# Performance work log

Hardware: AMD Instinct MI355X
Metric: run time of the kernel (lower is better)

## Reference

```python
import jax, jax.numpy as jnp
import numpy as np

H = 2048            # hidden_size
HK, HV = 16, 32     # num_k_heads, num_v_heads
DK, DV = 128, 128   # head dims
KEY_DIM = HK * DK   # 2048
VAL_DIM = HV * DV   # 4096
CONV_DIM = 2 * KEY_DIM + VAL_DIM  # 8192
KW = 4              # conv kernel width
CS = 64             # chunk size
B, S = 2, 4096
EPS = 1e-6


def setup_inputs() -> dict:
    key = jax.random.key(0)
    ks = jax.random.split(key, 8)
    sc = lambda n: 1.0 / np.sqrt(n)
    return {
        "hidden_states": jax.random.normal(ks[0], (B, S, H), jnp.float32),
        "W_qkvz": jax.random.normal(ks[1], (H, 2 * KEY_DIM + 2 * VAL_DIM), jnp.float32) * sc(H),
        "W_ba": jax.random.normal(ks[2], (H, 2 * HV), jnp.float32) * sc(H),
        "conv_w": jax.random.normal(ks[3], (CONV_DIM, KW), jnp.float32) * sc(KW),
        "A_log": jnp.log(jax.random.uniform(ks[4], (HV,), jnp.float32, 1.0, 16.0)),
        "dt_bias": jax.random.normal(ks[5], (HV,), jnp.float32) * 0.1,
        "norm_weight": jnp.ones((DV,), jnp.float32),
        "W_out": jax.random.normal(ks[6], (VAL_DIM, H), jnp.float32) * sc(VAL_DIM),
    }


def l2norm(x, eps=1e-6):
    return x * jax.lax.rsqrt(jnp.sum(x * x, -1, keepdims=True) + eps)


def chunk_gated_delta_rule(q, k, v, g, beta):
    # q,k: (B,S,HV,DK); v: (B,S,HV,DV); g,beta: (B,S,HV). S divisible by CS.
    q = l2norm(q)
    k = l2norm(k)
    tr = lambda x: jnp.swapaxes(x, 1, 2).astype(jnp.float32)  # -> (B,H,S,...)
    q, k, v = tr(q), tr(k), tr(v)
    g = jnp.swapaxes(g, 1, 2).astype(jnp.float32)
    beta = jnp.swapaxes(beta, 1, 2).astype(jnp.float32)
    q = q * (1.0 / np.sqrt(DK))
    nc = S // CS
    rs = lambda x: x.reshape(B, HV, nc, CS, x.shape[-1])
    v_beta = v * beta[..., None]
    k_beta = k * beta[..., None]
    q, k, v, k_beta, v_beta = map(rs, (q, k, v, k_beta, v_beta))
    g = jnp.cumsum(g.reshape(B, HV, nc, CS), -1)
    tril = jnp.tril(jnp.ones((CS, CS), bool))
    diff = g[..., :, None] - g[..., None, :]
    decay = jnp.exp(jnp.where(tril, diff, 0.0)) * tril  # (B,H,nc,CS,CS)
    # strictly-lower A; the original sequential loop computes T = (I - A)^{-1}
    A = -jnp.tril(jnp.einsum('bhcid,bhcjd->bhcij', k_beta, k) * decay, -1)
    eye = jnp.eye(CS, dtype=jnp.float32)
    T = jax.scipy.linalg.solve_triangular(
        eye - A, jnp.broadcast_to(eye, A.shape), lower=True, unit_diagonal=True)
    v_t = jnp.einsum('bhcij,bhcjd->bhcid', T, v_beta)
    k_cumdecay = jnp.einsum('bhcij,bhcjd->bhcid', T, k_beta * jnp.exp(g)[..., None])
    strict_low = jnp.tril(jnp.ones((CS, CS), jnp.float32), -1)

    def step(state, xs):
        q_i, k_i, v_i, kc_i, g_i, dm_i = xs  # (B,H,CS,*)
        attn = jnp.einsum('bhid,bhjd->bhij', q_i, k_i) * dm_i * strict_low
        v_new = v_i - kc_i @ state
        out = (q_i * jnp.exp(g_i)[..., None]) @ state + attn @ v_new
        g_last = g_i[..., -1]
        state = state * jnp.exp(g_last)[..., None, None] + jnp.einsum(
            'bhcd,bhcv->bhdv', k_i * jnp.exp(g_last[..., None] - g_i)[..., None], v_new)
        return state, out

    S0 = jnp.zeros((B, HV, DK, DV), jnp.float32)
    mv = lambda x: jnp.moveaxis(x, 2, 0)  # chunk axis first for scan
    _, outs = jax.lax.scan(step, S0, (mv(q), mv(k), mv(v_t), mv(k_cumdecay), mv(g), mv(decay)))
    out = jnp.moveaxis(outs, 0, 2).reshape(B, HV, S, DV)
    return jnp.swapaxes(out, 1, 2)  # (B,S,HV,DV)


def reference(hidden_states, W_qkvz, W_ba, conv_w, A_log, dt_bias, norm_weight, W_out):
    r = HV // HK
    qkvz = hidden_states @ W_qkvz                     # (B,S,2*KEY+2*VAL)
    ba = hidden_states @ W_ba                         # (B,S,2*HV)
    qkvz = qkvz.reshape(B, S, HK, 2 * DK + 2 * r * DV)
    q, k, v, z = jnp.split(qkvz, [DK, 2 * DK, 2 * DK + r * DV], axis=-1)
    v = v.reshape(B, S, HV, DV)
    z = z.reshape(B, S, HV, DV)
    ba = ba.reshape(B, S, HK, 2 * r)
    b, a = jnp.split(ba, [r], axis=-1)
    b = b.reshape(B, S, HV)
    a = a.reshape(B, S, HV)
    # fused causal depthwise conv + silu over [q|k|v]
    mixed = jnp.concatenate([q.reshape(B, S, -1), k.reshape(B, S, -1), v.reshape(B, S, -1)], -1)
    x = jnp.swapaxes(mixed, 1, 2)                     # (B, CONV_DIM, S)
    xp = jnp.pad(x, ((0, 0), (0, 0), (KW - 1, 0)))
    conv = sum(conv_w[:, j][None, :, None] * xp[:, :, j:j + S] for j in range(KW))
    conv = jax.nn.silu(conv)
    qkv = jnp.swapaxes(conv, 1, 2)
    q, k, v = jnp.split(qkv, [KEY_DIM, 2 * KEY_DIM], axis=-1)
    q = q.reshape(B, S, HK, DK)
    k = k.reshape(B, S, HK, DK)
    v = v.reshape(B, S, HV, DV)
    beta = jax.nn.sigmoid(b)
    g = -jnp.exp(A_log) * jax.nn.softplus(a + dt_bias)
    q = jnp.repeat(q, r, axis=2)
    k = jnp.repeat(k, r, axis=2)
    core = chunk_gated_delta_rule(q, k, v, g, beta)   # (B,S,HV,DV)
    # gated RMSNorm over head_v_dim
    cf = core.astype(jnp.float32)
    var = jnp.mean(cf * cf, -1, keepdims=True)
    core = cf * jax.lax.rsqrt(var + EPS) * norm_weight
    core = core * jax.nn.silu(z.astype(jnp.float32))
    return core.reshape(B, S, VAL_DIM) @ W_out        # (B,S,H)
```

## Files before the change

kernel.cpp:

```cpp
#include <hip/hip_runtime.h>
#include <cstdint>
#include <cstddef>


typedef _Float16 half_t;
typedef _Float16 half2_t __attribute__((ext_vector_type(2)));
typedef _Float16 half4_t __attribute__((ext_vector_type(4)));
typedef _Float16 half8   __attribute__((ext_vector_type(8)));
typedef float    f32x4   __attribute__((ext_vector_type(4)));

#define MFMA16(a, b, c) __builtin_amdgcn_mfma_f32_16x16x32_f16((a), (b), (c), 0, 0, 0)

#define AS1 __attribute__((address_space(1)))
#define AS3 __attribute__((address_space(3)))

__device__ __forceinline__ void gload16(void* lds, const void* g) {
    __builtin_amdgcn_global_load_lds((AS1 void*)(g), (AS3 void*)(lds), 16, 0, 0);
}

__device__ __forceinline__ void at_wr(float* AT, int i, int j, float v) {
    *(float*)((char*)AT + i * 256 + ((j * 4) ^ ((i & 7) << 4))) = v;
}
__device__ __forceinline__ half8 frag64(const half_t* base, int row, int koff) {
    return *(const half8*)((const char*)base + row * 128 + ((koff * 2) ^ ((row & 7) << 4)));
}
__device__ __forceinline__ void w64(half_t* base, int row, int col, float v) {
    *(half_t*)((char*)base + row * 128 + ((col * 2) ^ ((row & 7) << 4))) = (half_t)v;
}
__device__ __forceinline__ half8 frag128(const half_t* base, int row, int koff) {
    return *(const half8*)((const char*)base + row * 256 + ((koff * 2) ^ ((row & 7) << 4)));
}

__global__ __launch_bounds__(256) void cast_h_k(const float* __restrict__ src,
                                                half_t* __restrict__ dst) {
    long i = (long)blockIdx.x * 256 + threadIdx.x;
    f32x4 v = *(const f32x4*)(src + i * 4);
    half4_t h;
    h[0] = (half_t)v[0]; h[1] = (half_t)v[1]; h[2] = (half_t)v[2]; h[3] = (half_t)v[3];
    *(half4_t*)(dst + i * 4) = h;
}

__global__ __launch_bounds__(256) void build_w1t_k(const float* __restrict__ Wq,
                                                   const float* __restrict__ Wba,
                                                   half_t* __restrict__ W1T) {
    __shared__ half_t tile[32][33];
    int n0 = blockIdx.x * 32, k0 = blockIdx.y * 32;
    int tx = threadIdx.x & 31, ty = threadIdx.x >> 5;
#pragma unroll
    for (int t = 0; t < 4; ++t) {
        int k = k0 + ty + t * 8, n = n0 + tx;
        float v = 0.f;
        if (n < 2048) {
            int kh = n >> 7, d = n & 127;
            v = Wq[(long)k * 12288 + kh * 768 + d];
        } else if (n < 4096) {
            int n2 = n - 2048; int kh = n2 >> 7, d = n2 & 127;
            v = Wq[(long)k * 12288 + kh * 768 + 128 + d];
        } else if (n < 8192) {
            int n3 = n - 4096; int vh = n3 >> 7, d = n3 & 127;
            int kh = vh >> 1, jj = vh & 1;
            v = Wq[(long)k * 12288 + kh * 768 + 256 + jj * 128 + d];
        } else if (n < 12288) {
            int n4 = n - 8192; int vh = n4 >> 7, d = n4 & 127;
            int kh = vh >> 1, jj = vh & 1;
            v = Wq[(long)k * 12288 + kh * 768 + 512 + jj * 128 + d];
        } else if (n < 12352) {
            v = Wba[(long)k * 64 + (n - 12288)];
        }
        tile[ty + t * 8][tx] = (half_t)v;
    }
    __syncthreads();
#pragma unroll
    for (int t = 0; t < 4; ++t) {
        int n = n0 + ty + t * 8, k = k0 + tx;
        W1T[(long)n * 2048 + k] = tile[tx][ty + t * 8];
    }
}

__global__ __launch_bounds__(256) void build_wot_k(const float* __restrict__ Wo,
                                                   half_t* __restrict__ WoT) {
    __shared__ half_t tile[32][33];
    int n0 = blockIdx.x * 32, k0 = blockIdx.y * 32;
    int tx = threadIdx.x & 31, ty = threadIdx.x >> 5;
#pragma unroll
    for (int t = 0; t < 4; ++t) {
        int k = k0 + ty + t * 8, n = n0 + tx;
        tile[ty + t * 8][tx] = (half_t)Wo[(long)k * 2048 + n];
    }
    __syncthreads();
#pragma unroll
    for (int t = 0; t < 4; ++t) {
        int n = n0 + ty + t * 8, k = k0 + tx;
        WoT[(long)n * 4096 + k] = tile[tx][ty + t * 8];
    }
}

template <int OUT_F16>
__global__ __launch_bounds__(512, 2) void gemm256_k(const half_t* __restrict__ A,
                                                    const half_t* __restrict__ Bt,
                                                    void* __restrict__ C,
                                                    int K, int ldc,
                                                    int nwgM, int nwgN) {
    __shared__ half_t LA[2][2][8192];
    __shared__ half_t LB[2][2][8192];
    const int tid = threadIdx.x, lane = tid & 63, w = tid >> 6;
    const int lo = lane & 15, hi = lane >> 4;
    const int wm = w >> 2, wn = w & 3;
    const int nwg = gridDim.x, q = nwg >> 3, bid = blockIdx.x;
    const int swz = (bid & 7) * q + (bid >> 3);
    const int grp = 8 * nwgN;
    const int gid = swz / grp;
    const int rem = swz - gid * grp;
    const int fm = gid * 8;
    const int gsz = min(nwgM - fm, 8);
    const long tm = fm + rem % gsz;
    const long tn = rem / gsz;
    const long Kb = (long)K * 2;
    const char* Ab = (const char*)A + tm * 256 * Kb;
    const char* Bb = (const char*)Bt + tn * 256 * Kb;
    const int scol = ((lane & 7) << 4) ^ ((lane >> 3) << 4);
    const int srow = lane >> 3;
    const int s0 = w * 2, s1 = w * 2 + 1;

    auto stA = [&](int kt, int h) {
        char* hb = (char*)&LA[kt & 1][h][0];
        const char* gb = Ab + (long)(h * 128) * Kb + (long)kt * 128;
        gload16(hb + s0 * 1024, gb + (long)(s0 * 8 + srow) * Kb + scol);
        gload16(hb + s1 * 1024, gb + (long)(s1 * 8 + srow) * Kb + scol);
    };
    auto stB = [&](int kt, int h) {
        char* hb = (char*)&LB[kt & 1][h][0];
        const char* gb = Bb + (long)(h * 128) * Kb + (long)kt * 128;
        gload16(hb + s0 * 1024, gb + (long)(s0 * 8 + srow) * Kb + scol);
        gload16(hb + s1 * 1024, gb + (long)(s1 * 8 + srow) * Kb + scol);
    };
    auto rdA = [&](int p, int mt, int ks) -> half8 {
        int r = mt * 16 + lo;
        return *(const half8*)((const char*)&LA[p][wm][0] + r * 128 +
                               ((ks * 64 + hi * 16) ^ ((r & 7) << 4)));
    };
    auto rdB = [&](int p, int nt, int ks) -> half8 {
        int r = (wn & 1) * 64 + nt * 16 + lo;
        return *(const half8*)((const char*)&LB[p][wn >> 1][0] + r * 128 +
                               ((ks * 64 + hi * 16) ^ ((r & 7) << 4)));
    };

    f32x4 acc[8][4] = {};
    half8 af[4][2], bfa[2][2], bfb[2][2];

    auto ldsA4 = [&](int p, int mbase) {
#pragma unroll
        for (int mt = 0; mt < 4; ++mt) {
            af[mt][0] = rdA(p, mbase + mt, 0);
            af[mt][1] = rdA(p, mbase + mt, 1);
        }
    };
    auto ldsB2 = [&](int p, int nbase, half8 (&dst)[2][2]) {
#pragma unroll
        for (int nt = 0; nt < 2; ++nt) {
            dst[nt][0] = rdB(p, nbase + nt, 0);
            dst[nt][1] = rdB(p, nbase + nt, 1);
        }
    };
    auto quad = [&](const half8 (&bq)[2][2], int mo, int no) {
        __builtin_amdgcn_s_setprio(1);
#pragma unroll
        for (int mt = 0; mt < 4; ++mt)
#pragma unroll
            for (int nt = 0; nt < 2; ++nt) {
                acc[mo + mt][no + nt] = MFMA16(af[mt][0], bq[nt][0], acc[mo + mt][no + nt]);
                acc[mo + mt][no + nt] = MFMA16(af[mt][1], bq[nt][1], acc[mo + mt][no + nt]);
            }
        __builtin_amdgcn_s_setprio(0);
        __builtin_amdgcn_s_barrier();
    };

    const int nkt = K >> 6, niter = nkt >> 1;
    stA(0, 0); stA(0, 1); stB(0, 0); stB(0, 1);
    stA(1, 0); stB(1, 0); stB(1, 1);
    asm volatile("s_waitcnt vmcnt(6)" ::: "memory");
    __builtin_amdgcn_s_barrier();
    ldsB2(0, 0, bfa);

    for (int i = 0; i < niter; ++i) {
        const int k0 = 2 * i, k1 = 2 * i + 1;
        const bool sa = (k0 + 2 < nkt), sb = (k1 + 2 < nkt);
        ldsA4(0, 0);
        stA(k1, 1);
        __builtin_amdgcn_s_barrier();
        quad(bfa, 0, 0);
        ldsB2(0, 2, bfb);
        __builtin_amdgcn_s_barrier();
        quad(bfb, 0, 2);
        ldsA4(0, 4);
        if (sa) stB(k0 + 2, 0);
        __builtin_amdgcn_s_barrier();
        quad(bfa, 4, 0);
        if (sa) {
            stA(k0 + 2, 0); stB(k0 + 2, 1);
            asm volatile("s_waitcnt vmcnt(6)" ::: "memory");
        } else {
            asm volatile("s_waitcnt vmcnt(0)" ::: "memory");
        }
        ldsB2(1, 0, bfa);
        __builtin_amdgcn_s_barrier();
        quad(bfb, 4, 2);
        ldsA4(1, 0);
        if (sa) stA(k0 + 2, 1);
        __builtin_amdgcn_s_barrier();
        quad(bfa, 0, 0);
        ldsB2(1, 2, bfb);
        __builtin_amdgcn_s_barrier();
        quad(bfb, 0, 2);
        ldsA4(1, 4);
        if (sb) stB(k1 + 2, 0);
        __builtin_amdgcn_s_barrier();
        quad(bfa, 4, 0);
        if (sb) {
            stA(k1 + 2, 0); stB(k1 + 2, 1);
            asm volatile("s_waitcnt vmcnt(6)" ::: "memory");
        }
        if (i + 1 < niter) ldsB2(0, 0, bfa);
        __builtin_amdgcn_s_barrier();
        quad(bfb, 4, 2);
    }

    const long crow0 = tm * 256 + wm * 128 + hi * 4;
    const long ccol0 = tn * 256 + wn * 64 + lo;
#pragma unroll
    for (int mt = 0; mt < 8; ++mt)
#pragma unroll
        for (int nt = 0; nt < 4; ++nt)
#pragma unroll
            for (int e = 0; e < 4; ++e) {
                long row = crow0 + mt * 16 + e;
                long col = ccol0 + nt * 16;
                if (OUT_F16)
                    ((half_t*)C)[row * (long)ldc + col] = (half_t)acc[mt][nt][e];
                else
                    ((float*)C)[row * (long)ldc + col] = acc[mt][nt][e];
            }
}

__global__ __launch_bounds__(256) void ba_gemm_k(const half_t* __restrict__ A,
                                                 const half_t* __restrict__ Bt,
                                                 half_t* __restrict__ baH) {
    int tid = threadIdx.x, lane = tid & 63, w = tid >> 6;
    int lo = lane & 15, hi = lane >> 4;
    int mt = w >> 1, np = w & 1;
    long rb = (long)blockIdx.x * 32;
    f32x4 acc[2] = {};
#pragma unroll 4
    for (int kk = 0; kk < 64; ++kk) {
        half8 a = *(const half8*)(A + (rb + mt * 16 + lo) * 2048 + kk * 32 + hi * 8);
#pragma unroll
        for (int j = 0; j < 2; ++j) {
            half8 b = *(const half8*)(Bt + (long)(np * 32 + j * 16 + lo) * 2048 +
                                      kk * 32 + hi * 8);
            acc[j] = MFMA16(a, b, acc[j]);
        }
    }
#pragma unroll
    for (int j = 0; j < 2; ++j)
#pragma unroll
        for (int e = 0; e < 4; ++e)
            baH[(rb + mt * 16 + hi * 4 + e) * 64 + np * 32 + j * 16 + lo] =
                (half_t)acc[j][e];
}

__global__ __launch_bounds__(256) void conv_silu_k(const half_t* __restrict__ mixedH,
                                                   const float* __restrict__ conv_w,
                                                   half_t* __restrict__ qb,
                                                   half_t* __restrict__ kb,
                                                   half_t* __restrict__ vb) {
    const int ldm = 8320;
    int ch0 = (blockIdx.x * 256 + threadIdx.x) * 8;
    int b = blockIdx.y >> 5, sc = blockIdx.y & 31;
    int s0 = sc * 128;
    half_t* dptr;
    long dstr;
    if (ch0 < 2048)      { dptr = qb + ch0;          dstr = 2048; }
    else if (ch0 < 4096) { dptr = kb + (ch0 - 2048); dstr = 2048; }
    else                 { dptr = vb + (ch0 - 4096); dstr = 4096; }
    float w0[8], w1[8], w2[8], w3[8];
#pragma unroll
    for (int j = 0; j < 8; ++j) {
        f32x4 wv = *(const f32x4*)(conv_w + (ch0 + j) * 4);
        w0[j] = wv[0]; w1[j] = wv[1]; w2[j] = wv[2]; w3[j] = wv[3];
    }
    const half_t* src = mixedH + (long)b * 4096 * ldm + ch0;
    half8 x0 = {}, x1 = {}, x2 = {};
    if (s0 >= 3) {
        x0 = *(const half8*)(src + (long)(s0 - 3) * ldm);
        x1 = *(const half8*)(src + (long)(s0 - 2) * ldm);
        x2 = *(const half8*)(src + (long)(s0 - 1) * ldm);
    }
    for (int s = s0; s < s0 + 128; ++s) {
        half8 x3 = *(const half8*)(src + (long)s * ldm);
        half8 yv;
#pragma unroll
        for (int j = 0; j < 8; ++j) {
            float y = w0[j] * (float)x0[j] + w1[j] * (float)x1[j] +
                      w2[j] * (float)x2[j] + w3[j] * (float)x3[j];
            y = y / (1.f + __expf(-y));
            yv[j] = (half_t)y;
        }
        *(half8*)(dptr + ((long)b * 4096 + s) * dstr) = yv;
        x0 = x1; x1 = x2; x2 = x3;
    }
}

__global__ __launch_bounds__(256) void gate_beta_k(const half_t* __restrict__ baH,
                                                   const float* __restrict__ A_log,
                                                   const float* __restrict__ dt_bias,
                                                   float* __restrict__ beta,
                                                   float* __restrict__ gcum) {
    __shared__ float gs[32][64];
    int b = blockIdx.x >> 6, c = blockIdx.x & 63;
    for (int idx = threadIdx.x; idx < 2048; idx += 256) {
        int vh = idx & 31, i = idx >> 5;
        int kh = vh >> 1, j = vh & 1;
        long row = ((long)b * 4096 + c * 64 + i) * 64 + kh * 4;
        float bb = (float)baH[row + j];
        float aa = (float)baH[row + 2 + j];
        beta[((long)b * 4096 + c * 64 + i) * 32 + vh] = 1.f / (1.f + __expf(-bb));
        float x = aa + dt_bias[vh];
        float sp = (x > 15.f) ? x : log1pf(__expf(x));
        gs[vh][i] = -__expf(A_log[vh]) * sp;
    }
    __syncthreads();
    if (threadIdx.x < 32) {
        int vh = threadIdx.x;
        float cum = 0.f;
        float* gout = gcum + ((long)(b * 32 + vh)) * 4096 + c * 64;
        for (int i = 0; i < 64; ++i) { cum += gs[vh][i]; gout[i] = cum; }
    }
}

__global__ __launch_bounds__(256) void l2norm_k(half_t* __restrict__ qb,
                                                half_t* __restrict__ kb) {
    int w = threadIdx.x >> 6, lane = threadIdx.x & 63;
    long rid = (long)blockIdx.x * 4 + w;
    half_t* base;
    float sc;
    if (rid < 131072) { base = qb + rid * 128; sc = 0.08838834764831845f; }
    else              { base = kb + (rid - 131072) * 128; sc = 1.f; }
    half2_t hv = *(half2_t*)(base + lane * 2);
    float f0 = (float)hv[0], f1 = (float)hv[1];
    float ss = f0 * f0 + f1 * f1;
#pragma unroll
    for (int off = 32; off; off >>= 1) ss += __shfl_xor(ss, off);
    float r = rsqrtf(ss + 1e-6f) * sc;
    half2_t o; o[0] = (half_t)(f0 * r); o[1] = (half_t)(f1 * r);
    *(half2_t*)(base + lane * 2) = o;
}

__global__ __launch_bounds__(256) void phase1_k(const half_t* __restrict__ qb,
                                                const half_t* __restrict__ kb,
                                                const half_t* __restrict__ vb,
                                                const float* __restrict__ beta,
                                                const float* __restrict__ gcum,
                                                half_t* __restrict__ attnW,
                                                half_t* __restrict__ vtW,
                                                half_t* __restrict__ kcW) {
    __shared__ float AT[64 * 64];
    __shared__ half_t XT[256 * 64];
    __shared__ float gcS[64], betaS[64], egS[64];
    int blk = blockIdx.x;
    int c = blk & 63, vh = (blk >> 6) & 31, b = blk >> 11;
    int kh = vh >> 1;
    int tid = threadIdx.x, lane = tid & 63, w = tid >> 6, lo = lane & 15, hi = lane >> 4;
    long rowbase = (long)b * 4096 + c * 64;
    if (tid < 64) {
        float g = gcum[((long)(b * 32 + vh)) * 4096 + c * 64 + tid];
        gcS[tid] = g; egS[tid] = __expf(g);
        betaS[tid] = beta[(rowbase + tid) * 32 + vh];
    }
    const half_t* kR = kb + rowbase * 2048 + kh * 128;
    const half_t* qR = qb + rowbase * 2048 + kh * 128;
    f32x4 accG[4] = {}, accA[4] = {};
#pragma unroll
    for (int kt = 0; kt < 4; ++kt) {
        half8 ak = *(const half8*)(kR + (long)(w * 16 + lo) * 2048 + kt * 32 + hi * 8);
        half8 aq = *(const half8*)(qR + (long)(w * 16 + lo) * 2048 + kt * 32 + hi * 8);
#pragma unroll
        for (int n = 0; n < 4; ++n) {
            half8 bk = *(const half8*)(kR + (long)(n * 16 + lo) * 2048 + kt * 32 + hi * 8);
            accG[n] = MFMA16(ak, bk, accG[n]);
            accA[n] = MFMA16(aq, bk, accA[n]);
        }
    }
    __syncthreads();
    half_t* attnB = attnW + (long)blk * 4096;
#pragma unroll
    for (int n = 0; n < 4; ++n)
#pragma unroll
        for (int e = 0; e < 4; ++e) {
            int i = w * 16 + hi * 4 + e;
            int j = n * 16 + lo;
            float dec = (j < i) ? __expf(gcS[i] - gcS[j]) : 0.f;
            float av = (j < i) ? (-betaS[i] * accG[n][e] * dec) : (j == i ? 1.f : 0.f);
            at_wr(AT, i, j, av);
            attnB[(long)i * 64 + j] = (half_t)((j < i) ? accA[n][e] * dec : 0.f);
        }
    __syncthreads();
    if (w == 0) {
        float t[64];
#pragma unroll
        for (int i = 0; i < 64; ++i) t[i] = (lane == i) ? 1.f : 0.f;
#pragma unroll
        for (int i = 1; i < 64; ++i) {
            float a0 = 0.f, a1 = 0.f, a2 = 0.f, a3 = 0.f;
#pragma unroll
            for (int p0 = 0; p0 < i; p0 += 4) {
                f32x4 a4 = *(const f32x4*)((const char*)AT + i * 256 +
                                           ((p0 * 4) ^ ((i & 7) << 4)));
                if (p0 + 0 < i) a0 += a4[0] * t[p0 + 0];
                if (p0 + 1 < i) a1 += a4[1] * t[p0 + 1];
                if (p0 + 2 < i) a2 += a4[2] * t[p0 + 2];
                if (p0 + 3 < i) a3 += a4[3] * t[p0 + 3];
            }
            t[i] += (a0 + a1) + (a2 + a3);
        }
        half_t* TS = (half_t*)AT;
#pragma unroll
        for (int i = 0; i < 64; ++i)
            *(half_t*)((char*)TS + i * 128 + ((lane * 2) ^ ((i & 7) << 4))) = (half_t)t[i];
    } else {
        for (int idx = tid - 64; idx < 4096; idx += 192) {
            int p = idx >> 6, dp = idx & 63;
            float bb = betaS[p], be = betaS[p] * egS[p];
            half2_t vv = *(const half2_t*)(vb + (rowbase + p) * 4096 + vh * 128 + dp * 2);
            half2_t kk = *(const half2_t*)(kb + (rowbase + p) * 2048 + kh * 128 + dp * 2);
            w64(XT, dp * 2,       p, (float)vv[0] * bb);
            w64(XT, dp * 2 + 1,   p, (float)vv[1] * bb);
            w64(XT, 128 + dp * 2,     p, (float)kk[0] * be);
            w64(XT, 128 + dp * 2 + 1, p, (float)kk[1] * be);
        }
    }
    __syncthreads();
    const half_t* TS = (const half_t*)AT;
    f32x4 accO[4][4] = {};
#pragma unroll
    for (int kt = 0; kt < 2; ++kt) {
        half8 tf[4];
#pragma unroll
        for (int m = 0; m < 4; ++m) tf[m] = frag64(TS, m * 16 + lo, kt * 32 + hi * 8);
#pragma unroll
        for (int n = 0; n < 4; ++n) {
            half8 bx = frag64(XT, w * 64 + n * 16 + lo, kt * 32 + hi * 8);
#pragma unroll
            for (int m = 0; m < 4; ++m) accO[m][n] = MFMA16(tf[m], bx, accO[m][n]);
        }
    }
    long ob = (long)blk * 8192;
#pragma unroll
    for (int m = 0; m < 4; ++m)
#pragma unroll
        for (int n = 0; n < 4; ++n)
#pragma unroll
            for (int e = 0; e < 4; ++e) {
                int i = m * 16 + hi * 4 + e;
                int dc = w * 64 + n * 16 + lo;
                float v = accO[m][n][e];
                if (dc < 128) vtW[ob + (long)i * 128 + dc] = (half_t)v;
                else          kcW[ob + (long)i * 128 + dc - 128] = (half_t)(-v);
            }
}

struct P2Ops {
    half8 kcf[4], qf[4], k8[4];
    half8 atf[2];
    half_t vtv[8];
    float gm, gi, g63;
};

__global__ __launch_bounds__(256, 1) void phase2_k(const half_t* __restrict__ qb,
                                                   const half_t* __restrict__ kb,
                                                   const float* __restrict__ gcum,
                                                   const half_t* __restrict__ attnW,
                                                   const half_t* __restrict__ vtW,
                                                   const half_t* __restrict__ kcW,
                                                   half_t* __restrict__ coreH) {
    __shared__ half_t SHs[32 * 128];
    __shared__ half_t vnT[32 * 64];
    __shared__ half_t kdT[128 * 64];
    int blk = blockIdx.x;
    int bvh = blk & 63, js = blk >> 6;
    int vh = bvh & 31, b = bvh >> 5, kh = vh >> 1;
    int j0 = js * 32;
    int tid = threadIdx.x, lane = tid & 63, w = tid >> 6, lo = lane & 15, hi = lane >> 4;
    int ii = tid >> 2, dseg = tid & 3;
    int jm = w >> 1, dql = (w & 1) * 4;
    for (int idx = tid; idx < 32 * 128; idx += 256) SHs[idx] = (half_t)0.f;
    __syncthreads();
    const float* gbase = gcum + (long)bvh * 4096;

    auto loadops = [&](int c, P2Ops& o) {
        long pb = (long)bvh * 64 + c;
        const half_t* kcG = kcW + pb * 8192;
        const half_t* vtG = vtW + pb * 8192;
        const half_t* atG = attnW + pb * 4096;
        long rowbase = (long)b * 4096 + c * 64;
        const float* gp = gbase + c * 64;
#pragma unroll
        for (int kt = 0; kt < 4; ++kt) {
            o.kcf[kt] = *(const half8*)(kcG + (long)(w * 16 + lo) * 128 + kt * 32 + hi * 8);
            o.qf[kt] = *(const half8*)(qb + (rowbase + w * 16 + lo) * 2048 + kh * 128 +
                                       kt * 32 + hi * 8);
        }
#pragma unroll
        for (int kt2 = 0; kt2 < 2; ++kt2)
            o.atf[kt2] = *(const half8*)(atG + (long)(w * 16 + lo) * 64 + kt2 * 32 + hi * 8);
#pragma unroll
        for (int s = 0; s < 4; ++s)
            o.k8[s] = *(const half8*)(kb + (rowbase + ii) * 2048 + kh * 128 + dseg * 32 + s * 8);
#pragma unroll
        for (int n = 0; n < 2; ++n)
#pragma unroll
            for (int e = 0; e < 4; ++e)
                o.vtv[n * 4 + e] = vtG[(long)(w * 16 + hi * 4 + e) * 128 + j0 + n * 16 + lo];
        o.gm = gp[w * 16 + lo];
        o.gi = gp[ii];
        o.g63 = gp[63];
    };

    auto step = [&](int c, P2Ops& o, P2Ops& nx) {
        long rowbase = (long)b * 4096 + c * 64;
        loadops(c + 1 < 64 ? c + 1 : 63, nx);
        half8 bS[4][2];
#pragma unroll
        for (int kt = 0; kt < 4; ++kt) {
            bS[kt][0] = frag128(SHs, lo, kt * 32 + hi * 8);
            bS[kt][1] = frag128(SHs, 16 + lo, kt * 32 + hi * 8);
        }
        f32x4 accV[2];
#pragma unroll
        for (int n = 0; n < 2; ++n)
#pragma unroll
            for (int e = 0; e < 4; ++e) accV[n][e] = (float)o.vtv[n * 4 + e];
#pragma unroll
        for (int kt = 0; kt < 4; ++kt) {
            accV[0] = MFMA16(o.kcf[kt], bS[kt][0], accV[0]);
            accV[1] = MFMA16(o.kcf[kt], bS[kt][1], accV[1]);
        }
#pragma unroll
        for (int n = 0; n < 2; ++n) {
            int j = n * 16 + lo, i0 = w * 16 + hi * 4;
            half4_t h4;
            h4[0] = (half_t)accV[n][0]; h4[1] = (half_t)accV[n][1];
            h4[2] = (half_t)accV[n][2]; h4[3] = (half_t)accV[n][3];
            *(half4_t*)((char*)vnT + j * 128 + ((i0 * 2) ^ ((j & 7) << 4))) = h4;
        }
        {
            float ek = __expf(o.g63 - o.gi);
#pragma unroll
            for (int s = 0; s < 4; ++s)
#pragma unroll
                for (int e2 = 0; e2 < 8; ++e2)
                    w64(kdT, dseg * 32 + s * 8 + e2, ii, (float)o.k8[s][e2] * ek);
        }
        __syncthreads();
        float egm = __expf(o.gm);
        f32x4 accO[2] = {};
#pragma unroll
        for (int kt = 0; kt < 4; ++kt) {
            half8 aq;
#pragma unroll
            for (int e2 = 0; e2 < 8; ++e2) aq[e2] = (half_t)((float)o.qf[kt][e2] * egm);
            accO[0] = MFMA16(aq, bS[kt][0], accO[0]);
            accO[1] = MFMA16(aq, bS[kt][1], accO[1]);
        }
#pragma unroll
        for (int kt2 = 0; kt2 < 2; ++kt2) {
            half8 bV0 = frag64(vnT, lo, kt2 * 32 + hi * 8);
            half8 bV1 = frag64(vnT, 16 + lo, kt2 * 32 + hi * 8);
            accO[0] = MFMA16(o.atf[kt2], bV0, accO[0]);
            accO[1] = MFMA16(o.atf[kt2], bV1, accO[1]);
        }
        f32x4 accU[4] = {};
#pragma unroll
        for (int kt2 = 0; kt2 < 2; ++kt2) {
            half8 avn = frag64(vnT, jm * 16 + lo, kt2 * 32 + hi * 8);
#pragma unroll
            for (int dnn = 0; dnn < 4; ++dnn) {
                half8 bkd = frag64(kdT, (dql + dnn) * 16 + lo, kt2 * 32 + hi * 8);
                accU[dnn] = MFMA16(avn, bkd, accU[dnn]);
            }
        }
#pragma unroll
        for (int n = 0; n < 2; ++n)
#pragma unroll
            for (int e = 0; e < 4; ++e)
                coreH[(rowbase + w * 16 + hi * 4 + e) * 4096 + vh * 128 + j0 + n * 16 + lo] =
                    (half_t)accO[n][e];
        __syncthreads();
        float egl = __expf(o.g63);
#pragma unroll
        for (int dnn = 0; dnn < 4; ++dnn)
#pragma unroll
            for (int e = 0; e < 4; ++e) {
                int j = jm * 16 + hi * 4 + e;
                int d = (dql + dnn) * 16 + lo;
                char* p = (char*)SHs + j * 256 + ((d * 2) ^ ((j & 7) << 4));
                float old = (float)*(half_t*)p;
                *(half_t*)p = (half_t)(old * egl + accU[dnn][e]);
            }
        __syncthreads();
    };

    P2Ops opsA, opsB;
    loadops(0, opsA);
    for (int c = 0; c < 64; c += 2) {
        step(c, opsA, opsB);
        step(c + 1, opsB, opsA);
    }
}

__global__ __launch_bounds__(256) void normgate_k(half_t* __restrict__ coreH,
                                                  const half_t* __restrict__ zH,
                                                  const float* __restrict__ norm_w) {
    int w = threadIdx.x >> 6, lane = threadIdx.x & 63;
    long rid = (long)blockIdx.x * 4 + w;
    long bs = rid >> 5;
    int vh = rid & 31;
    half_t* cr = coreH + bs * 4096 + vh * 128;
    half2_t cv = *(half2_t*)(cr + lane * 2);
    float f0 = (float)cv[0], f1 = (float)cv[1];
    float ss = f0 * f0 + f1 * f1;
#pragma unroll
    for (int off = 32; off; off >>= 1) ss += __shfl_xor(ss, off);
    float rs = rsqrtf(ss * (1.f / 128.f) + 1e-6f);
    half2_t zz = *(const half2_t*)(zH + bs * 4096 + vh * 128 + lane * 2);
    float z0 = (float)zz[0], z1 = (float)zz[1];
    float s0 = z0 / (1.f + __expf(-z0)), s1 = z1 / (1.f + __expf(-z1));
    float w0 = norm_w[lane * 2], w1 = norm_w[lane * 2 + 1];
    half2_t o;
    o[0] = (half_t)(f0 * rs * w0 * s0);
    o[1] = (half_t)(f1 * rs * w1 * s1);
    *(half2_t*)(cr + lane * 2) = o;
}

extern "C" void kernel_launch(void* const* d_in, const int* in_sizes, int n_in,
                              void* d_out, int out_size, void* d_ws, size_t ws_size,
                              hipStream_t stream) {
    const float* hidden  = (const float*)d_in[0];
    const float* W_qkvz  = (const float*)d_in[1];
    const float* W_ba    = (const float*)d_in[2];
    const float* conv_w  = (const float*)d_in[3];
    const float* A_log   = (const float*)d_in[4];
    const float* dt_bias = (const float*)d_in[5];
    const float* norm_w  = (const float*)d_in[6];
    const float* W_out   = (const float*)d_in[7];
    float* out = (float*)d_out;

    char* ws = (char*)d_ws;
    const size_t MB = 1ull << 20;
    half_t* qb      = (half_t*)(ws + 0);
    half_t* kb      = (half_t*)(ws + 32 * MB);
    half_t* vb      = (half_t*)(ws + 64 * MB);
    float*  betaB   = (float*) (ws + 128 * MB);
    float*  gcum    = (float*) (ws + 129 * MB);
    half_t* WoT     = (half_t*)(ws + 130 * MB);
    half_t* zH      = (half_t*)(ws + 146 * MB);
    half_t* mixedH  = (half_t*)(ws + 210 * MB);
    half_t* attnW   = (half_t*)(ws + 210 * MB);
    half_t* vtW     = (half_t*)(ws + 242 * MB);
    half_t* kcW     = (half_t*)(ws + 306 * MB);
    half_t* baH     = (half_t*)(ws + 340 * MB);
    half_t* hiddenH = (half_t*)(ws + 0);
    half_t* W1T     = (half_t*)(ws + 32 * MB);
    half_t* coreH   = (half_t*)(ws + 64 * MB);
    (void)ws_size; (void)in_sizes; (void)n_in; (void)out_size;

    cast_h_k<<<16384, 256, 0, stream>>>(hidden, hiddenH);
    build_w1t_k<<<dim3(392, 64), 256, 0, stream>>>(W_qkvz, W_ba, W1T);
    build_wot_k<<<dim3(64, 128), 256, 0, stream>>>(W_out, WoT);
    gemm256_k<1><<<1024, 512, 0, stream>>>(hiddenH, W1T, mixedH, 2048, 8320, 32, 32);
    gemm256_k<1><<<512, 512, 0, stream>>>(hiddenH, W1T + (size_t)8192 * 2048, zH,
                                          2048, 4096, 32, 16);
    ba_gemm_k<<<256, 256, 0, stream>>>(hiddenH, W1T + (size_t)12288 * 2048, baH);
    conv_silu_k<<<dim3(4, 64), 256, 0, stream>>>(mixedH, conv_w, qb, kb, vb);
    gate_beta_k<<<128, 256, 0, stream>>>(baH, A_log, dt_bias, betaB, gcum);
    l2norm_k<<<65536, 256, 0, stream>>>(qb, kb);
    phase1_k<<<4096, 256, 0, stream>>>(qb, kb, vb, betaB, gcum, attnW, vtW, kcW);
    phase2_k<<<256, 256, 0, stream>>>(qb, kb, gcum, attnW, vtW, kcW, coreH);
    normgate_k<<<65536, 256, 0, stream>>>(coreH, zH, norm_w);
    gemm256_k<0><<<256, 512, 0, stream>>>(coreH, WoT, out, 4096, 2048, 32, 8);
}
```

Measured before the change: 1.289 ms.

## Fuse ba projection into qkv GEMM, l2norm into conv, use grid-stride elementwise kernels

The b/a projection columns move into the main mixed GEMM (width padded to 8448), which drops the separate ba_gemm kernel, and gate_beta now reads b/a straight from mixedH. The q/k l2norm and the q scaling are folded into the conv+silu kernel through a 16-lane shuffle reduction, which removes a full read/write pass over q and k. The conv kernel now uses more blocks with shorter sequence chunks, and the cast and normgate kernels become grid-stride loops with far fewer blocks. In exchange the GEMM computes 128 padding columns of zeros, and the conv kernel reloads 3 halo rows for each shorter chunk.

```diff
diff --git a/kernel.cpp b/kernel.cpp
--- a/kernel.cpp
+++ b/kernel.cpp
@@ -33,11 +33,13 @@
 
 __global__ __launch_bounds__(256) void cast_h_k(const float* __restrict__ src,
                                                 half_t* __restrict__ dst) {
-    long i = (long)blockIdx.x * 256 + threadIdx.x;
-    f32x4 v = *(const f32x4*)(src + i * 4);
-    half4_t h;
-    h[0] = (half_t)v[0]; h[1] = (half_t)v[1]; h[2] = (half_t)v[2]; h[3] = (half_t)v[3];
-    *(half4_t*)(dst + i * 4) = h;
+    const long n4 = (long)8192 * 2048 / 4;
+    for (long i = (long)blockIdx.x * 256 + threadIdx.x; i < n4; i += (long)gridDim.x * 256) {
+        f32x4 v = *(const f32x4*)(src + i * 4);
+        half4_t h;
+        h[0] = (half_t)v[0]; h[1] = (half_t)v[1]; h[2] = (half_t)v[2]; h[3] = (half_t)v[3];
+        *(half4_t*)(dst + i * 4) = h;
+    }
 }
 
 __global__ __launch_bounds__(256) void build_w1t_k(const float* __restrict__ Wq,
@@ -60,12 +62,12 @@
             int n3 = n - 4096; int vh = n3 >> 7, d = n3 & 127;
             int kh = vh >> 1, jj = vh & 1;
             v = Wq[(long)k * 12288 + kh * 768 + 256 + jj * 128 + d];
-        } else if (n < 12288) {
-            int n4 = n - 8192; int vh = n4 >> 7, d = n4 & 127;
+        } else if (n < 8256) {
+            v = Wba[(long)k * 64 + (n - 8192)];
+        } else if (n >= 8448) {
+            int n4 = n - 8448; int vh = n4 >> 7, d = n4 & 127;
             int kh = vh >> 1, jj = vh & 1;
             v = Wq[(long)k * 12288 + kh * 768 + 512 + jj * 128 + d];
-        } else if (n < 12352) {
-            v = Wba[(long)k * 64 + (n - 12288)];
         }
         tile[ty + t * 8][tx] = (half_t)v;
     }
@@ -242,46 +244,23 @@
             }
 }
 
-__global__ __launch_bounds__(256) void ba_gemm_k(const half_t* __restrict__ A,
-                                                 const half_t* __restrict__ Bt,
-                                                 half_t* __restrict__ baH) {
-    int tid = threadIdx.x, lane = tid & 63, w = tid >> 6;
-    int lo = lane & 15, hi = lane >> 4;
-    int mt = w >> 1, np = w & 1;
-    long rb = (long)blockIdx.x * 32;
-    f32x4 acc[2] = {};
-#pragma unroll 4
-    for (int kk = 0; kk < 64; ++kk) {
-        half8 a = *(const half8*)(A + (rb + mt * 16 + lo) * 2048 + kk * 32 + hi * 8);
-#pragma unroll
-        for (int j = 0; j < 2; ++j) {
-            half8 b = *(const half8*)(Bt + (long)(np * 32 + j * 16 + lo) * 2048 +
-                                      kk * 32 + hi * 8);
-            acc[j] = MFMA16(a, b, acc[j]);
-        }
-    }
-#pragma unroll
-    for (int j = 0; j < 2; ++j)
-#pragma unroll
-        for (int e = 0; e < 4; ++e)
-            baH[(rb + mt * 16 + hi * 4 + e) * 64 + np * 32 + j * 16 + lo] =
-                (half_t)acc[j][e];
-}
-
 __global__ __launch_bounds__(256) void conv_silu_k(const half_t* __restrict__ mixedH,
                                                    const float* __restrict__ conv_w,
                                                    half_t* __restrict__ qb,
                                                    half_t* __restrict__ kb,
                                                    half_t* __restrict__ vb) {
-    const int ldm = 8320;
-    int ch0 = (blockIdx.x * 256 + threadIdx.x) * 8;
-    int b = blockIdx.y >> 5, sc = blockIdx.y & 31;
-    int s0 = sc * 128;
+    const int ldm = 8448;
+    int bx = blockIdx.x;
+    int ch0 = (bx * 256 + threadIdx.x) * 8;
+    int b = blockIdx.y >> 7, sc = blockIdx.y & 127;
+    int s0 = sc * 32;
     half_t* dptr;
     long dstr;
-    if (ch0 < 2048)      { dptr = qb + ch0;          dstr = 2048; }
-    else if (ch0 < 4096) { dptr = kb + (ch0 - 2048); dstr = 2048; }
-    else                 { dptr = vb + (ch0 - 4096); dstr = 4096; }
+    float nsc = 1.f;
+    bool donorm = (bx < 2);
+    if (bx == 0)      { dptr = qb + ch0;          dstr = 2048; nsc = 0.08838834764831845f; }
+    else if (bx == 1) { dptr = kb + (ch0 - 2048); dstr = 2048; }
+    else              { dptr = vb + (ch0 - 4096); dstr = 4096; }
     float w0[8], w1[8], w2[8], w3[8];
 #pragma unroll
     for (int j = 0; j < 8; ++j) {
@@ -295,22 +274,37 @@
         x1 = *(const half8*)(src + (long)(s0 - 2) * ldm);
         x2 = *(const half8*)(src + (long)(s0 - 1) * ldm);
     }
-    for (int s = s0; s < s0 + 128; ++s) {
+    for (int s = s0; s < s0 + 32; ++s) {
         half8 x3 = *(const half8*)(src + (long)s * ldm);
+        float y[8];
+        float ss = 0.f;
+#pragma unroll
+        for (int j = 0; j < 8; ++j) {
+            float t = w0[j] * (float)x0[j] + w1[j] * (float)x1[j] +
+                      w2[j] * (float)x2[j] + w3[j] * (float)x3[j];
+            t = t / (1.f + __expf(-t));
+            y[j] = t;
+            ss += t * t;
+        }
         half8 yv;
-#pragma unroll
-        for (int j = 0; j < 8; ++j) {
-            float y = w0[j] * (float)x0[j] + w1[j] * (float)x1[j] +
-                      w2[j] * (float)x2[j] + w3[j] * (float)x3[j];
-            y = y / (1.f + __expf(-y));
-            yv[j] = (half_t)y;
+        if (donorm) {
+            ss += __shfl_xor(ss, 1);
+            ss += __shfl_xor(ss, 2);
+            ss += __shfl_xor(ss, 4);
+            ss += __shfl_xor(ss, 8);
+            float r = rsqrtf(ss + 1e-6f) * nsc;
+#pragma unroll
+            for (int j = 0; j < 8; ++j) yv[j] = (half_t)(y[j] * r);
+        } else {
+#pragma unroll
+            for (int j = 0; j < 8; ++j) yv[j] = (half_t)y[j];
         }
         *(half8*)(dptr + ((long)b * 4096 + s) * dstr) = yv;
         x0 = x1; x1 = x2; x2 = x3;
     }
 }
 
-__global__ __launch_bounds__(256) void gate_beta_k(const half_t* __restrict__ baH,
+__global__ __launch_bounds__(256) void gate_beta_k(const half_t* __restrict__ mixedH,
                                                    const float* __restrict__ A_log,
                                                    const float* __restrict__ dt_bias,
                                                    float* __restrict__ beta,
@@ -320,9 +314,9 @@
     for (int idx = threadIdx.x; idx < 2048; idx += 256) {
         int vh = idx & 31, i = idx >> 5;
         int kh = vh >> 1, j = vh & 1;
-        long row = ((long)b * 4096 + c * 64 + i) * 64 + kh * 4;
-        float bb = (float)baH[row + j];
-        float aa = (float)baH[row + 2 + j];
+        long row = ((long)b * 4096 + c * 64 + i) * 8448 + 8192 + kh * 4;
+        float bb = (float)mixedH[row + j];
+        float aa = (float)mixedH[row + 2 + j];
         beta[((long)b * 4096 + c * 64 + i) * 32 + vh] = 1.f / (1.f + __expf(-bb));
         float x = aa + dt_bias[vh];
         float sp = (x > 15.f) ? x : log1pf(__expf(x));
@@ -335,24 +329,6 @@
         float* gout = gcum + ((long)(b * 32 + vh)) * 4096 + c * 64;
         for (int i = 0; i < 64; ++i) { cum += gs[vh][i]; gout[i] = cum; }
     }
-}
-
-__global__ __launch_bounds__(256) void l2norm_k(half_t* __restrict__ qb,
-                                                half_t* __restrict__ kb) {
-    int w = threadIdx.x >> 6, lane = threadIdx.x & 63;
-    long rid = (long)blockIdx.x * 4 + w;
-    half_t* base;
-    float sc;
-    if (rid < 131072) { base = qb + rid * 128; sc = 0.08838834764831845f; }
-    else              { base = kb + (rid - 131072) * 128; sc = 1.f; }
-    half2_t hv = *(half2_t*)(base + lane * 2);
-    float f0 = (float)hv[0], f1 = (float)hv[1];
-    float ss = f0 * f0 + f1 * f1;
-#pragma unroll
-    for (int off = 32; off; off >>= 1) ss += __shfl_xor(ss, off);
-    float r = rsqrtf(ss + 1e-6f) * sc;
-    half2_t o; o[0] = (half_t)(f0 * r); o[1] = (half_t)(f1 * r);
-    *(half2_t*)(base + lane * 2) = o;
 }
 
 __global__ __launch_bounds__(256) void phase1_k(const half_t* __restrict__ qb,
@@ -621,24 +597,25 @@
                                                   const half_t* __restrict__ zH,
                                                   const float* __restrict__ norm_w) {
     int w = threadIdx.x >> 6, lane = threadIdx.x & 63;
-    long rid = (long)blockIdx.x * 4 + w;
-    long bs = rid >> 5;
-    int vh = rid & 31;
-    half_t* cr = coreH + bs * 4096 + vh * 128;
-    half2_t cv = *(half2_t*)(cr + lane * 2);
-    float f0 = (float)cv[0], f1 = (float)cv[1];
-    float ss = f0 * f0 + f1 * f1;
-#pragma unroll
-    for (int off = 32; off; off >>= 1) ss += __shfl_xor(ss, off);
-    float rs = rsqrtf(ss * (1.f / 128.f) + 1e-6f);
-    half2_t zz = *(const half2_t*)(zH + bs * 4096 + vh * 128 + lane * 2);
-    float z0 = (float)zz[0], z1 = (float)zz[1];
-    float s0 = z0 / (1.f + __expf(-z0)), s1 = z1 / (1.f + __expf(-z1));
     float w0 = norm_w[lane * 2], w1 = norm_w[lane * 2 + 1];
-    half2_t o;
-    o[0] = (half_t)(f0 * rs * w0 * s0);
-    o[1] = (half_t)(f1 * rs * w1 * s1);
-    *(half2_t*)(cr + lane * 2) = o;
+    for (long rid = (long)blockIdx.x * 4 + w; rid < 262144; rid += (long)gridDim.x * 4) {
+        long bs = rid >> 5;
+        int vh = rid & 31;
+        half_t* cr = coreH + bs * 4096 + vh * 128;
+        half2_t cv = *(half2_t*)(cr + lane * 2);
+        float f0 = (float)cv[0], f1 = (float)cv[1];
+        float ss = f0 * f0 + f1 * f1;
+#pragma unroll
+        for (int off = 32; off; off >>= 1) ss += __shfl_xor(ss, off);
+        float rs = rsqrtf(ss * (1.f / 128.f) + 1e-6f);
+        half2_t zz = *(const half2_t*)(zH + bs * 4096 + vh * 128 + lane * 2);
+        float z0 = (float)zz[0], z1 = (float)zz[1];
+        float s0 = z0 / (1.f + __expf(-z0)), s1 = z1 / (1.f + __expf(-z1));
+        half2_t o;
+        o[0] = (half_t)(f0 * rs * w0 * s0);
+        o[1] = (half_t)(f1 * rs * w1 * s1);
+        *(half2_t*)(cr + lane * 2) = o;
+    }
 }
 
 extern "C" void kernel_launch(void* const* d_in, const int* in_sizes, int n_in,
@@ -667,24 +644,21 @@
     half_t* attnW   = (half_t*)(ws + 210 * MB);
     half_t* vtW     = (half_t*)(ws + 242 * MB);
     half_t* kcW     = (half_t*)(ws + 306 * MB);
-    half_t* baH     = (half_t*)(ws + 340 * MB);
     half_t* hiddenH = (half_t*)(ws + 0);
     half_t* W1T     = (half_t*)(ws + 32 * MB);
     half_t* coreH   = (half_t*)(ws + 64 * MB);
     (void)ws_size; (void)in_sizes; (void)n_in; (void)out_size;
 
-    cast_h_k<<<16384, 256, 0, stream>>>(hidden, hiddenH);
+    cast_h_k<<<2048, 256, 0, stream>>>(hidden, hiddenH);
     build_w1t_k<<<dim3(392, 64), 256, 0, stream>>>(W_qkvz, W_ba, W1T);
     build_wot_k<<<dim3(64, 128), 256, 0, stream>>>(W_out, WoT);
-    gemm256_k<1><<<1024, 512, 0, stream>>>(hiddenH, W1T, mixedH, 2048, 8320, 32, 32);
-    gemm256_k<1><<<512, 512, 0, stream>>>(hiddenH, W1T + (size_t)8192 * 2048, zH,
+    gemm256_k<1><<<1056, 512, 0, stream>>>(hiddenH, W1T, mixedH, 2048, 8448, 32, 33);
+    gemm256_k<1><<<512, 512, 0, stream>>>(hiddenH, W1T + (size_t)8448 * 2048, zH,
                                           2048, 4096, 32, 16);
-    ba_gemm_k<<<256, 256, 0, stream>>>(hiddenH, W1T + (size_t)12288 * 2048, baH);
-    conv_silu_k<<<dim3(4, 64), 256, 0, stream>>>(mixedH, conv_w, qb, kb, vb);
-    gate_beta_k<<<128, 256, 0, stream>>>(baH, A_log, dt_bias, betaB, gcum);
-    l2norm_k<<<65536, 256, 0, stream>>>(qb, kb);
+    conv_silu_k<<<dim3(4, 256), 256, 0, stream>>>(mixedH, conv_w, qb, kb, vb);
+    gate_beta_k<<<128, 256, 0, stream>>>(mixedH, A_log, dt_bias, betaB, gcum);
     phase1_k<<<4096, 256, 0, stream>>>(qb, kb, vb, betaB, gcum, attnW, vtW, kcW);
     phase2_k<<<256, 256, 0, stream>>>(qb, kb, gcum, attnW, vtW, kcW, coreH);
-    normgate_k<<<65536, 256, 0, stream>>>(coreH, zH, norm_w);
+    normgate_k<<<4096, 256, 0, stream>>>(coreH, zH, norm_w);
     gemm256_k<0><<<256, 512, 0, stream>>>(coreH, WoT, out, 4096, 2048, 32, 8);
 }
```

New measurement: 1.223 ms. 5.1% less time.
